# Performance work log

Measured on AMD Instinct MI355X. Metric: run time of the kernel, lower is better.

Reference implementation:

```python
import jax, jax.numpy as jnp
import numpy as np

B, N, D = 2, 1024, 1024
H = 4
KD = 512          # key_dim = d_model * 0.5
VD = 1024         # value_dim = d_model
DK = KD // H      # 128 head_qk_dim
DV = VD // H      # 256 head_v_dim
LR = 16           # gate_low_rank_dim
GLN = 16.0        # gate_logit_normalizer
EPS = 1e-5


def setup_inputs() -> dict:
    key = jax.random.key(0)
    ks = jax.random.split(key, 10)
    s = 0.02
    return {
        "x": jax.random.normal(ks[0], (B, N, D), jnp.float32),
        "Wq": jax.random.normal(ks[1], (D, KD), jnp.float32) * s,
        "Wk": jax.random.normal(ks[2], (D, KD), jnp.float32) * s,
        "Wv": jax.random.normal(ks[3], (D, VD), jnp.float32) * s,
        "Wg": jax.random.normal(ks[4], (D, VD), jnp.float32) * s,
        "Wgk1": jax.random.normal(ks[5], (D, LR), jnp.float32) * s,
        "Wgk2": jax.random.normal(ks[6], (LR, KD), jnp.float32) * s,
        "bgk2": jax.random.normal(ks[7], (KD,), jnp.float32) * s,
        "Wout": jax.random.normal(ks[8], (VD, D), jnp.float32) * s,
        "rms_w": jnp.ones((DV,), jnp.float32),
    }


def _split_heads(t, h):
    b, n, hd = t.shape
    return t.reshape(b, n, h, hd // h).transpose(0, 2, 1, 3)  # b h n d


def _gla_scan(q, k, v, g):
    # q,k: [b,h,n,dk]; v: [b,h,n,dv]; g: [b,h,n,dk] (log-decay)
    b, h, n, dk = q.shape
    dv = v.shape[-1]
    qT = jnp.moveaxis(q, 2, 0)  # [n,b,h,dk]
    kT = jnp.moveaxis(k, 2, 0)
    vT = jnp.moveaxis(v, 2, 0)
    gT = jnp.moveaxis(g, 2, 0)

    def step(S, inp):
        qt, kt, vt, gt = inp
        # S_t = diag(exp(g_t)) S_{t-1} + k_t v_t^T ; o_t = q_t S_t
        S = S * jnp.exp(gt)[..., None] + kt[..., None] * vt[..., None, :]
        ot = jnp.einsum('bhk,bhkv->bhv', qt, S)
        return S, ot

    S0 = jnp.zeros((b, h, dk, dv), q.dtype)
    _, o = jax.lax.scan(step, S0, (qT, kT, vT, gT))
    return jnp.moveaxis(o, 0, 2)  # [b,h,n,dv]


def reference(x, Wq, Wk, Wv, Wg, Wgk1, Wgk2, bgk2, Wout, rms_w):
    q = _split_heads(x @ Wq, H)
    k = _split_heads(x @ Wk, H)
    v = _split_heads(x @ Wv, H)
    g = jax.nn.log_sigmoid((x @ Wgk1) @ Wgk2 + bgk2) / GLN
    g = jnp.maximum(g, -3.0)  # chunk mode clamp
    g = _split_heads(g, H)
    o = _gla_scan(q, k, v, g)               # [b,h,n,dv]
    o = o.transpose(0, 2, 1, 3)             # [b,n,h,dv]
    # RMSNorm over head_v_dim
    o = o * jax.lax.rsqrt(jnp.mean(o * o, axis=-1, keepdims=True) + EPS) * rms_w
    o = o.reshape(o.shape[0], o.shape[1], VD)
    o = o * jax.nn.silu(x @ Wg)
    return o @ Wout
```

## Files before the change

### kernel.cpp

```cpp
#include <hip/hip_runtime.h>
#include <math.h>


typedef __attribute__((ext_vector_type(4))) float vf4;
typedef __attribute__((ext_vector_type(4))) unsigned int vu4;
typedef __attribute__((ext_vector_type(8))) short short8;

#define DEVI static __device__ __forceinline__
DEVI vf4 vzero() { vf4 x = {0.f, 0.f, 0.f, 0.f}; return x; }

DEVI float bf2f(unsigned int u) {
  union { unsigned int i; float f; } c; c.i = u << 16; return c.f;
}
DEVI unsigned short f2bf(float f) {
  union { float f; unsigned int i; } c; c.f = f;
  unsigned int i = c.i;
  return (unsigned short)((i + 0x7fffu + ((i >> 16) & 1u)) >> 16);
}
DEVI void unpack8(vu4 r, float* f) {
  f[0] = bf2f(r.x & 0xffffu); f[1] = bf2f(r.x >> 16);
  f[2] = bf2f(r.y & 0xffffu); f[3] = bf2f(r.y >> 16);
  f[4] = bf2f(r.z & 0xffffu); f[5] = bf2f(r.z >> 16);
  f[6] = bf2f(r.w & 0xffffu); f[7] = bf2f(r.w >> 16);
}
DEVI vu4 pack8(const float* f) {
  vu4 o;
  o.x = (unsigned int)f2bf(f[0]) | ((unsigned int)f2bf(f[1]) << 16);
  o.y = (unsigned int)f2bf(f[2]) | ((unsigned int)f2bf(f[3]) << 16);
  o.z = (unsigned int)f2bf(f[4]) | ((unsigned int)f2bf(f[5]) << 16);
  o.w = (unsigned int)f2bf(f[6]) | ((unsigned int)f2bf(f[7]) << 16);
  return o;
}

__global__ __launch_bounds__(256)
void prep_k(const float* __restrict__ Wq, const float* __restrict__ Wk,
            const float* __restrict__ Wv, const float* __restrict__ Wg,
            const float* __restrict__ Wo, const float* __restrict__ X,
            unsigned short* __restrict__ wqT, unsigned short* __restrict__ wkT,
            unsigned short* __restrict__ wvT, unsigned short* __restrict__ wgT,
            unsigned short* __restrict__ woT, unsigned short* __restrict__ xb) {
  __shared__ float T[64][65];
  const int ct = blockIdx.x, kt = blockIdx.y;
  const int t = threadIdx.x;
  const int r = t >> 2, s = t & 3;
  if (ct >= 64) {
    const int rt = ct - 64;
    const size_t base = (size_t)(rt * 64 + r) * 1024 + kt * 64 + s * 16;
    float f[16];
    *(vf4*)&f[0]  = *(const vf4*)(X + base);
    *(vf4*)&f[4]  = *(const vf4*)(X + base + 4);
    *(vf4*)&f[8]  = *(const vf4*)(X + base + 8);
    *(vf4*)&f[12] = *(const vf4*)(X + base + 12);
    *(vu4*)(xb + base) = pack8(f);
    *(vu4*)(xb + base + 8) = pack8(f + 8);
    return;
  }
  const float* W; unsigned short* O; int N; int cb;
  if (ct < 8)       { W = Wq; O = wqT; N = 512;  cb = ct; }
  else if (ct < 16) { W = Wk; O = wkT; N = 512;  cb = ct - 8; }
  else if (ct < 32) { W = Wv; O = wvT; N = 1024; cb = ct - 16; }
  else if (ct < 48) { W = Wg; O = wgT; N = 1024; cb = ct - 32; }
  else              { W = Wo; O = woT; N = 1024; cb = ct - 48; }
  const float* src = W + (size_t)(kt * 64 + r) * N + cb * 64 + s * 16;
#pragma unroll
  for (int u = 0; u < 4; ++u) {
    vf4 v4 = *(const vf4*)(src + u * 4);
    T[r][s * 16 + u * 4 + 0] = v4.x;
    T[r][s * 16 + u * 4 + 1] = v4.y;
    T[r][s * 16 + u * 4 + 2] = v4.z;
    T[r][s * 16 + u * 4 + 3] = v4.w;
  }
  __syncthreads();
  unsigned int pk[8];
#pragma unroll
  for (int u = 0; u < 8; ++u) {
    unsigned int lo = f2bf(T[s * 16 + 2 * u][r]);
    unsigned int hi = f2bf(T[s * 16 + 2 * u + 1][r]);
    pk[u] = lo | (hi << 16);
  }
  unsigned short* dst = O + (size_t)(cb * 64 + r) * 1024 + kt * 64 + s * 16;
  *(vu4*)dst = *(vu4*)&pk[0];
  *(vu4*)(dst + 8) = *(vu4*)&pk[4];
}

__global__ __launch_bounds__(256)
void proj_mfma_k(const unsigned short* __restrict__ xb,
                 const unsigned short* __restrict__ wqT, const unsigned short* __restrict__ wkT,
                 const unsigned short* __restrict__ wvT, const unsigned short* __restrict__ wgT,
                 unsigned short* __restrict__ qb, unsigned short* __restrict__ kb,
                 unsigned short* __restrict__ vb, unsigned short* __restrict__ sgb) {
  __shared__ __align__(16) unsigned short As[64 * 72];
  __shared__ __align__(16) unsigned short Bs[128 * 72];
  const int t = threadIdx.x;
  const int m0 = blockIdx.y << 6;
  const int nt = blockIdx.x;
  const unsigned short* WT; int n0; int kind;
  if (nt < 4)       { WT = wqT; n0 = nt * 128;        kind = 0; }
  else if (nt < 8)  { WT = wkT; n0 = (nt - 4) * 128;  kind = 1; }
  else if (nt < 16) { WT = wvT; n0 = (nt - 8) * 128;  kind = 2; }
  else              { WT = wgT; n0 = (nt - 16) * 128; kind = 3; }

  const int w = t >> 6, lane = t & 63;
  const int wm = (w >> 1) * 32, wn = (w & 1) * 64;
  const int qd = lane >> 4, m = lane & 15;

  vf4 acc[2][4];
#pragma unroll
  for (int i = 0; i < 2; ++i)
#pragma unroll
    for (int j = 0; j < 4; ++j) acc[i][j] = vzero();

  for (int k0 = 0; k0 < 1024; k0 += 64) {
    __syncthreads();
#pragma unroll
    for (int u2 = 0; u2 < 2; ++u2) {
      const int id = t + (u2 << 8);
      const int row = id >> 3, kg = id & 7;
      vu4 ra = *(const vu4*)(xb + (size_t)(m0 + row) * 1024 + k0 + kg * 8);
      *(vu4*)&As[row * 72 + kg * 8] = ra;
    }
#pragma unroll
    for (int u2 = 0; u2 < 4; ++u2) {
      const int id = t + (u2 << 8);
      const int row = id >> 3, kg = id & 7;
      vu4 rb = *(const vu4*)(WT + (size_t)(n0 + row) * 1024 + k0 + kg * 8);
      *(vu4*)&Bs[row * 72 + kg * 8] = rb;
    }
    __syncthreads();
#pragma unroll
    for (int ks = 0; ks < 2; ++ks) {
      short8 af[2], bf[4];
#pragma unroll
      for (int i = 0; i < 2; ++i)
        af[i] = *(const short8*)&As[(wm + i * 16 + m) * 72 + ks * 32 + qd * 8];
#pragma unroll
      for (int j = 0; j < 4; ++j)
        bf[j] = *(const short8*)&Bs[(wn + j * 16 + m) * 72 + ks * 32 + qd * 8];
#pragma unroll
      for (int i = 0; i < 2; ++i)
#pragma unroll
        for (int j = 0; j < 4; ++j)
          acc[i][j] = __builtin_amdgcn_mfma_f32_16x16x32_bf16(af[i], bf[j], acc[i][j], 0, 0, 0);
    }
  }
#pragma unroll
  for (int i = 0; i < 2; ++i) {
#pragma unroll
    for (int j = 0; j < 4; ++j) {
#pragma unroll
      for (int r = 0; r < 4; ++r) {
        const int grow = m0 + wm + i * 16 + qd * 4 + r;
        const int gcol = n0 + wn + j * 16 + m;
        float val = acc[i][j][r];
        if (kind == 0)      qb[(size_t)grow * 512 + gcol] = f2bf(val);
        else if (kind == 1) kb[(size_t)grow * 512 + gcol] = f2bf(val);
        else if (kind == 2) vb[(size_t)grow * 1024 + gcol] = f2bf(val);
        else {
          val = val / (1.f + expf(-val));
          sgb[(size_t)grow * 1024 + gcol] = f2bf(val);
        }
      }
    }
  }
}

__global__ __launch_bounds__(256)
void out_mfma_k(const unsigned short* __restrict__ Ab,
                const unsigned short* __restrict__ woT, float* __restrict__ Y) {
  __shared__ __align__(16) unsigned short As[64 * 72];
  __shared__ __align__(16) unsigned short Bs[128 * 72];
  const int t = threadIdx.x;
  const int m0 = blockIdx.y << 6;
  const int n0 = blockIdx.x << 7;
  const int w = t >> 6, lane = t & 63;
  const int wm = (w >> 1) * 32, wn = (w & 1) * 64;
  const int qd = lane >> 4, m = lane & 15;

  vf4 acc[2][4];
#pragma unroll
  for (int i = 0; i < 2; ++i)
#pragma unroll
    for (int j = 0; j < 4; ++j) acc[i][j] = vzero();

  for (int k0 = 0; k0 < 1024; k0 += 64) {
    __syncthreads();
#pragma unroll
    for (int u2 = 0; u2 < 2; ++u2) {
      const int id = t + (u2 << 8);
      const int row = id >> 3, kg = id & 7;
      vu4 ra = *(const vu4*)(Ab + (size_t)(m0 + row) * 1024 + k0 + kg * 8);
      *(vu4*)&As[row * 72 + kg * 8] = ra;
    }
#pragma unroll
    for (int u2 = 0; u2 < 4; ++u2) {
      const int id = t + (u2 << 8);
      const int row = id >> 3, kg = id & 7;
      vu4 rb = *(const vu4*)(woT + (size_t)(n0 + row) * 1024 + k0 + kg * 8);
      *(vu4*)&Bs[row * 72 + kg * 8] = rb;
    }
    __syncthreads();
#pragma unroll
    for (int ks = 0; ks < 2; ++ks) {
      short8 af[2], bf[4];
#pragma unroll
      for (int i = 0; i < 2; ++i)
        af[i] = *(const short8*)&As[(wm + i * 16 + m) * 72 + ks * 32 + qd * 8];
#pragma unroll
      for (int j = 0; j < 4; ++j)
        bf[j] = *(const short8*)&Bs[(wn + j * 16 + m) * 72 + ks * 32 + qd * 8];
#pragma unroll
      for (int i = 0; i < 2; ++i)
#pragma unroll
        for (int j = 0; j < 4; ++j)
          acc[i][j] = __builtin_amdgcn_mfma_f32_16x16x32_bf16(af[i], bf[j], acc[i][j], 0, 0, 0);
    }
  }
#pragma unroll
  for (int i = 0; i < 2; ++i)
#pragma unroll
    for (int j = 0; j < 4; ++j)
#pragma unroll
      for (int r = 0; r < 4; ++r) {
        const int grow = m0 + wm + i * 16 + qd * 4 + r;
        const int gcol = n0 + wn + j * 16 + m;
        Y[(size_t)grow * 1024 + gcol] = acc[i][j][r];
      }
}

__global__ __launch_bounds__(64)
void lowrank_k(const float* __restrict__ X, const float* __restrict__ W1,
               float* __restrict__ xl) {
  const int row = blockIdx.x;
  const int t = threadIdx.x;
  float acc[16];
#pragma unroll
  for (int c2 = 0; c2 < 16; ++c2) acc[c2] = 0.f;
  const float* xp = X + (size_t)row * 1024 + t * 16;
  float xv[16];
#pragma unroll
  for (int u = 0; u < 4; ++u)
    *(vf4*)&xv[u * 4] = *(const vf4*)(xp + u * 4);
#pragma unroll
  for (int j = 0; j < 16; ++j) {
    const float* wp = W1 + (size_t)(t * 16 + j) * 16;
    float wv[16];
#pragma unroll
    for (int u = 0; u < 4; ++u)
      *(vf4*)&wv[u * 4] = *(const vf4*)(wp + u * 4);
#pragma unroll
    for (int c2 = 0; c2 < 16; ++c2) acc[c2] = fmaf(xv[j], wv[c2], acc[c2]);
  }
#pragma unroll
  for (int mm = 1; mm < 64; mm <<= 1) {
#pragma unroll
    for (int c2 = 0; c2 < 16; ++c2) acc[c2] += __shfl_xor(acc[c2], mm, 64);
  }
  if (t == 0) {
#pragma unroll
    for (int c2 = 0; c2 < 16; ++c2) xl[(size_t)row * 16 + c2] = acc[c2];
  }
}

__global__ __launch_bounds__(256)
void gate_scan_k(const float* __restrict__ xl, const float* __restrict__ W2,
                 const float* __restrict__ bias,
                 unsigned short* __restrict__ q, unsigned short* __restrict__ k,
                 float* __restrict__ ebtot) {
  const int t = threadIdx.x;
  const int w = t >> 6, lane = t & 63;
  const int wid = blockIdx.x * 4 + w;
  const int kt = wid & 31;
  const int c = (wid >> 5) & 15;
  const int b = wid >> 9;
  const int kbase = kt * 16;
  const size_t rowbase = (size_t)b * 1024 + c * 64;

  const float* xp = xl + (rowbase + lane) * 16;
  float xv[16];
#pragma unroll
  for (int u = 0; u < 4; ++u)
    *(vf4*)&xv[u * 4] = *(const vf4*)(xp + u * 4);

  const size_t a = (rowbase + lane) * 512 + kbase;
  vu4 qr0 = *(const vu4*)(q + a), qr1 = *(const vu4*)(q + a + 8);
  vu4 kr0 = *(const vu4*)(k + a), kr1 = *(const vu4*)(k + a + 8);
  float qf[16], kf[16];
  unpack8(qr0, qf); unpack8(qr1, qf + 8);
  unpack8(kr0, kf); unpack8(kr1, kf + 8);

  float gf[16];
#pragma unroll
  for (int cc = 0; cc < 16; ++cc) {
    const int col = kbase + cc;
    float z = bias[col];
#pragma unroll
    for (int j = 0; j < 16; ++j) z = fmaf(xv[j], W2[j * 512 + col], z);
    float ls = fminf(z, 0.f) - log1pf(expf(-fabsf(z)));
    float g = fmaxf(ls * (1.f / 16.f), -3.f);
#pragma unroll
    for (int d = 1; d < 64; d <<= 1) {
      float up = __shfl_up(g, d, 64);
      if (lane >= d) g += up;
    }
    qf[cc] *= expf(g);
    kf[cc] *= expf(fminf(-g, 80.f));
    gf[cc] = g;
  }
  *(vu4*)(q + a) = pack8(qf);
  *(vu4*)(q + a + 8) = pack8(qf + 8);
  *(vu4*)(k + a) = pack8(kf);
  *(vu4*)(k + a + 8) = pack8(kf + 8);
  if (lane == 63) {
    float* ep = ebtot + ((size_t)b * 16 + c) * 512 + kbase;
#pragma unroll
    for (int cc = 0; cc < 16; ++cc) ep[cc] = expf(gf[cc]);
  }
}

__global__ __launch_bounds__(256)
void intra_kv_k(const unsigned short* __restrict__ q16, const unsigned short* __restrict__ k16,
                const unsigned short* __restrict__ v, float* __restrict__ o,
                unsigned short* __restrict__ ST) {
  __shared__ __align__(16) unsigned short Qs[64 * 136];
  __shared__ __align__(16) unsigned short Ks[64 * 136];
  __shared__ __align__(16) unsigned short Kt[128 * 68];
  __shared__ __align__(16) unsigned short Vt[128 * 68];
  __shared__ __align__(16) unsigned short Asb[64 * 68];
  const int t = threadIdx.x;
  const int vh = blockIdx.x, c = blockIdx.y, bh = blockIdx.z;
  const int b = bh >> 2, h = bh & 3;
  const size_t rowbase = (size_t)b * 1024 + c * 64;

#pragma unroll
  for (int u2 = 0; u2 < 4; ++u2) {
    const int id = t + (u2 << 8);
    const int row = id >> 4, kg = id & 15;
    vu4 rq = *(const vu4*)(q16 + (rowbase + row) * 512 + h * 128 + kg * 8);
    *(vu4*)&Qs[row * 136 + kg * 8] = rq;
    vu4 rk = *(const vu4*)(k16 + (rowbase + row) * 512 + h * 128 + kg * 8);
    *(vu4*)&Ks[row * 136 + kg * 8] = rk;
    const unsigned short* kp = (const unsigned short*)&rk;
#pragma unroll
    for (int u = 0; u < 8; ++u)
      Kt[(kg * 8 + u) * 68 + row] = kp[u];
    vu4 rv = *(const vu4*)(v + (rowbase + row) * 1024 + h * 256 + vh * 128 + kg * 8);
    const unsigned short* vp = (const unsigned short*)&rv;
#pragma unroll
    for (int u = 0; u < 8; ++u)
      Vt[(kg * 8 + u) * 68 + row] = vp[u];
  }
  __syncthreads();

  const int w = t >> 6, lane = t & 63;
  const int qd = lane >> 4, m = lane & 15;

  {
    short8 af[4];
#pragma unroll
    for (int kf = 0; kf < 4; ++kf)
      af[kf] = *(const short8*)&Qs[(w * 16 + m) * 136 + kf * 32 + qd * 8];
    vf4 acc[4];
#pragma unroll
    for (int jt = 0; jt < 4; ++jt) acc[jt] = vzero();
#pragma unroll
    for (int jt = 0; jt < 4; ++jt)
#pragma unroll
      for (int kf = 0; kf < 4; ++kf) {
        short8 bfr = *(const short8*)&Ks[(jt * 16 + m) * 136 + kf * 32 + qd * 8];
        acc[jt] = __builtin_amdgcn_mfma_f32_16x16x32_bf16(af[kf], bfr, acc[jt], 0, 0, 0);
      }
#pragma unroll
    for (int jt = 0; jt < 4; ++jt)
#pragma unroll
      for (int r = 0; r < 4; ++r) {
        const int i = w * 16 + qd * 4 + r;
        const int j = jt * 16 + m;
        Asb[i * 68 + j] = f2bf((j <= i) ? acc[jt][r] : 0.f);
      }
  }
  __syncthreads();

  {
    vf4 acc2[4][2];
#pragma unroll
    for (int mt = 0; mt < 4; ++mt) { acc2[mt][0] = vzero(); acc2[mt][1] = vzero(); }
#pragma unroll
    for (int kf = 0; kf < 2; ++kf) {
      short8 bf0 = *(const short8*)&Vt[(w * 32 + m) * 68 + kf * 32 + qd * 8];
      short8 bf1 = *(const short8*)&Vt[(w * 32 + 16 + m) * 68 + kf * 32 + qd * 8];
#pragma unroll
      for (int mt = 0; mt < 4; ++mt) {
        short8 af = *(const short8*)&Asb[(mt * 16 + m) * 68 + kf * 32 + qd * 8];
        acc2[mt][0] = __builtin_amdgcn_mfma_f32_16x16x32_bf16(af, bf0, acc2[mt][0], 0, 0, 0);
        acc2[mt][1] = __builtin_amdgcn_mfma_f32_16x16x32_bf16(af, bf1, acc2[mt][1], 0, 0, 0);
      }
    }
#pragma unroll
    for (int mt = 0; mt < 4; ++mt)
#pragma unroll
      for (int nt = 0; nt < 2; ++nt)
#pragma unroll
        for (int r = 0; r < 4; ++r) {
          const int i = mt * 16 + qd * 4 + r;
          const int vc = h * 256 + vh * 128 + w * 32 + nt * 16 + m;
          o[(rowbase + i) * 1024 + vc] = acc2[mt][nt][r];
        }
  }

  {
    short8 af3[2][2];
#pragma unroll
    for (int mt = 0; mt < 2; ++mt)
#pragma unroll
      for (int kf = 0; kf < 2; ++kf)
        af3[mt][kf] = *(const short8*)&Vt[(w * 32 + mt * 16 + m) * 68 + kf * 32 + qd * 8];
#pragma unroll
    for (int nt = 0; nt < 8; ++nt) {
      vf4 a0 = vzero(), a1 = vzero();
#pragma unroll
      for (int kf = 0; kf < 2; ++kf) {
        short8 bfr = *(const short8*)&Kt[(nt * 16 + m) * 68 + kf * 32 + qd * 8];
        a0 = __builtin_amdgcn_mfma_f32_16x16x32_bf16(af3[0][kf], bfr, a0, 0, 0, 0);
        a1 = __builtin_amdgcn_mfma_f32_16x16x32_bf16(af3[1][kf], bfr, a1, 0, 0, 0);
      }
      const size_t sbase = (size_t)(bh * 16 + c) * 256 + vh * 128 + w * 32;
#pragma unroll
      for (int r = 0; r < 4; ++r) {
        ST[(sbase + qd * 4 + r) * 128 + nt * 16 + m] = f2bf(a0[r]);
        ST[(sbase + 16 + qd * 4 + r) * 128 + nt * 16 + m] = f2bf(a1[r]);
      }
    }
  }
}

__global__ __launch_bounds__(256)
void state_scan_k(unsigned short* __restrict__ ST, const float* __restrict__ ebtot) {
  const int idx = blockIdx.x * 256 + threadIdx.x;
  const int kg = idx & 15;
  const int vv = (idx >> 4) & 255;
  const int bh = idx >> 12;
  const int b = bh >> 2, h = bh & 3;
  float s[8];
#pragma unroll
  for (int u = 0; u < 8; ++u) s[u] = 0.f;
  for (int c = 0; c < 16; ++c) {
    unsigned short* p = ST + ((size_t)(bh * 16 + c) * 256 + vv) * 128 + kg * 8;
    const float* ep = ebtot + ((size_t)b * 16 + c) * 512 + h * 128 + kg * 8;
    float e[8];
    *(vf4*)&e[0] = *(const vf4*)ep;
    *(vf4*)&e[4] = *(const vf4*)(ep + 4);
    float kv[8];
    unpack8(*(const vu4*)p, kv);
    *(vu4*)p = pack8(s);
#pragma unroll
    for (int u = 0; u < 8; ++u) s[u] = (s[u] + kv[u]) * e[u];
  }
}

__global__ __launch_bounds__(256)
void o_inter_k(const unsigned short* __restrict__ q16, const unsigned short* __restrict__ ST,
               float* __restrict__ o) {
  __shared__ __align__(16) unsigned short Qs[64 * 136];
  __shared__ __align__(16) unsigned short Ss[128 * 136];
  const int t = threadIdx.x;
  const int vt = blockIdx.x, c = blockIdx.y, bh = blockIdx.z;
  const int b = bh >> 2, h = bh & 3;
  const size_t rowbase = (size_t)b * 1024 + c * 64;

#pragma unroll
  for (int u2 = 0; u2 < 4; ++u2) {
    const int id = t + (u2 << 8);
    const int row = id >> 4, kg = id & 15;
    *(vu4*)&Qs[row * 136 + kg * 8] =
        *(const vu4*)(q16 + (rowbase + row) * 512 + h * 128 + kg * 8);
  }
#pragma unroll
  for (int u2 = 0; u2 < 8; ++u2) {
    const int id = t + (u2 << 8);
    const int vrow = id >> 4, kg = id & 15;
    *(vu4*)&Ss[vrow * 136 + kg * 8] =
        *(const vu4*)(ST + ((size_t)(bh * 16 + c) * 256 + vt * 128 + vrow) * 128 + kg * 8);
  }
  __syncthreads();

  const int w = t >> 6, lane = t & 63;
  const int qd = lane >> 4, m = lane & 15;
  short8 af[4];
#pragma unroll
  for (int kf = 0; kf < 4; ++kf)
    af[kf] = *(const short8*)&Qs[(w * 16 + m) * 136 + kf * 32 + qd * 8];
#pragma unroll
  for (int nt = 0; nt < 8; ++nt) {
    vf4 acc = vzero();
#pragma unroll
    for (int kf = 0; kf < 4; ++kf) {
      short8 bfr = *(const short8*)&Ss[(nt * 16 + m) * 136 + kf * 32 + qd * 8];
      acc = __builtin_amdgcn_mfma_f32_16x16x32_bf16(af[kf], bfr, acc, 0, 0, 0);
    }
    float* base = o + (rowbase + w * 16 + qd * 4) * 1024 + h * 256 + vt * 128 + nt * 16 + m;
#pragma unroll
    for (int r = 0; r < 4; ++r)
      base[(size_t)r * 1024] += acc[r];
  }
}

__global__ __launch_bounds__(256)
void norm_gate_k(const float* __restrict__ o, const float* __restrict__ rmsw,
                 const unsigned short* __restrict__ sg,
                 unsigned short* __restrict__ ob) {
  __shared__ float red[4];
  const int grp = blockIdx.x;
  const int row = grp >> 2, h = grp & 3;
  const int t = threadIdx.x;
  const size_t idx = (size_t)row * 1024 + h * 256 + t;
  const float val = o[idx];
  float ss = val * val;
#pragma unroll
  for (int mm = 1; mm < 64; mm <<= 1) ss += __shfl_xor(ss, mm, 64);
  if ((t & 63) == 0) red[t >> 6] = ss;
  __syncthreads();
  const float tot = red[0] + red[1] + red[2] + red[3];
  const float scale = rsqrtf(tot * (1.f / 256.f) + 1e-5f);
  ob[idx] = f2bf(val * scale * rmsw[t] * bf2f((unsigned int)sg[idx]));
}

extern "C" void kernel_launch(void* const* d_in, const int* in_sizes, int n_in,
                              void* d_out, int out_size, void* d_ws, size_t ws_size,
                              hipStream_t stream) {
  const float* x    = (const float*)d_in[0];
  const float* Wq   = (const float*)d_in[1];
  const float* Wk   = (const float*)d_in[2];
  const float* Wv   = (const float*)d_in[3];
  const float* Wg   = (const float*)d_in[4];
  const float* Wgk1 = (const float*)d_in[5];
  const float* Wgk2 = (const float*)d_in[6];
  const float* bgk2 = (const float*)d_in[7];
  const float* Wout = (const float*)d_in[8];
  const float* rmsw = (const float*)d_in[9];

  const size_t MB = 1u << 20;
  char* w = (char*)d_ws;
  unsigned short* qb16   = (unsigned short*)(w);
  unsigned short* kb16   = (unsigned short*)(w + 2 * MB);
  unsigned short* vbuf   = (unsigned short*)(w + 4 * MB);
  unsigned short* sgbuf  = (unsigned short*)(w + 8 * MB);
  float*          obuf   = (float*)(w + 12 * MB);
  char*           sreg   = w + 20 * MB;
  unsigned short* xb     = (unsigned short*)sreg;
  unsigned short* STbuf  = (unsigned short*)sreg;
  unsigned short* obuf_b = (unsigned short*)sreg;
  float*          xlbuf  = (float*)(w + 28 * MB);
  float*          ebbuf  = (float*)(w + 28 * MB + 131072);
  unsigned short* wqT    = (unsigned short*)(w + 29 * MB);
  unsigned short* wkT    = (unsigned short*)(w + 30 * MB);
  unsigned short* wvT    = (unsigned short*)(w + 31 * MB);
  unsigned short* wgT    = (unsigned short*)(w + 33 * MB);
  unsigned short* woT    = (unsigned short*)(w + 35 * MB);

  prep_k<<<dim3(96, 16), 256, 0, stream>>>(Wq, Wk, Wv, Wg, Wout, x,
                                           wqT, wkT, wvT, wgT, woT, xb);
  lowrank_k<<<2048, 64, 0, stream>>>(x, Wgk1, xlbuf);
  proj_mfma_k<<<dim3(24, 32), 256, 0, stream>>>(xb, wqT, wkT, wvT, wgT, qb16, kb16, vbuf, sgbuf);
  gate_scan_k<<<256, 256, 0, stream>>>(xlbuf, Wgk2, bgk2, qb16, kb16, ebbuf);
  intra_kv_k<<<dim3(2, 16, 8), 256, 0, stream>>>(qb16, kb16, vbuf, obuf, STbuf);
  state_scan_k<<<128, 256, 0, stream>>>(STbuf, ebbuf);
  o_inter_k<<<dim3(2, 16, 8), 256, 0, stream>>>(qb16, STbuf, obuf);
  norm_gate_k<<<8192, 256, 0, stream>>>(obuf, rmsw, sgbuf, obuf_b);
  out_mfma_k<<<dim3(8, 32), 256, 0, stream>>>(obuf_b, woT, (float*)d_out);
}
```

Baseline: 192.3 us.

## Use direct global-to-LDS loads with XOR swizzle and larger projection GEMM tile

Both the projection and output GEMMs now stage tiles with global_load_lds 16-byte direct-to-LDS loads instead of going through VGPRs. The padded LDS layout is replaced by an XOR-swizzled 64-wide layout to avoid bank conflicts. The projection GEMM tile grows from 64x128 to 128x128 with a 4x4 accumulator array per wave, halving the grid. This aims to cut register traffic and raise data reuse, at the cost of more registers per wave and fewer blocks for the projection kernel.

New measurement: 194.2 us. Within noise of the previous version (+1.0%).

```diff
diff --git a/kernel.cpp b/kernel.cpp
--- a/kernel.cpp
+++ b/kernel.cpp
@@ -30,6 +30,13 @@
   o.z = (unsigned int)f2bf(f[4]) | ((unsigned int)f2bf(f[5]) << 16);
   o.w = (unsigned int)f2bf(f[6]) | ((unsigned int)f2bf(f[7]) << 16);
   return o;
+}
+
+DEVI void gld16(const unsigned short* g, unsigned short* l) {
+  __builtin_amdgcn_global_load_lds(
+      (const __attribute__((address_space(1))) unsigned int*)g,
+      (__attribute__((address_space(3))) unsigned int*)l,
+      16, 0, 0);
 }
 
 __global__ __launch_bounds__(256)
@@ -89,62 +96,58 @@
                  const unsigned short* __restrict__ wvT, const unsigned short* __restrict__ wgT,
                  unsigned short* __restrict__ qb, unsigned short* __restrict__ kb,
                  unsigned short* __restrict__ vb, unsigned short* __restrict__ sgb) {
-  __shared__ __align__(16) unsigned short As[64 * 72];
-  __shared__ __align__(16) unsigned short Bs[128 * 72];
-  const int t = threadIdx.x;
-  const int m0 = blockIdx.y << 6;
+  __shared__ __align__(16) unsigned short As[128 * 64];
+  __shared__ __align__(16) unsigned short Bs[128 * 64];
+  const int t = threadIdx.x;
+  const int m0 = blockIdx.y << 7;
   const int nt = blockIdx.x;
   const unsigned short* WT; int n0; int kind;
-  if (nt < 4)       { WT = wqT; n0 = nt * 128;        kind = 0; }
-  else if (nt < 8)  { WT = wkT; n0 = (nt - 4) * 128;  kind = 1; }
-  else if (nt < 16) { WT = wvT; n0 = (nt - 8) * 128;  kind = 2; }
-  else              { WT = wgT; n0 = (nt - 16) * 128; kind = 3; }
+  if (nt < 4)       { WT = wqT; n0 = nt << 7;        kind = 0; }
+  else if (nt < 8)  { WT = wkT; n0 = (nt - 4) << 7;  kind = 1; }
+  else if (nt < 16) { WT = wvT; n0 = (nt - 8) << 7;  kind = 2; }
+  else              { WT = wgT; n0 = (nt - 16) << 7; kind = 3; }
 
   const int w = t >> 6, lane = t & 63;
-  const int wm = (w >> 1) * 32, wn = (w & 1) * 64;
+  const int wm = (w >> 1) << 6, wn = (w & 1) << 6;
   const int qd = lane >> 4, m = lane & 15;
-
-  vf4 acc[2][4];
-#pragma unroll
-  for (int i = 0; i < 2; ++i)
+  const int srow = lane >> 3;
+  const int scol = ((lane & 7) ^ srow) << 3;
+
+  vf4 acc[4][4];
+#pragma unroll
+  for (int i = 0; i < 4; ++i)
 #pragma unroll
     for (int j = 0; j < 4; ++j) acc[i][j] = vzero();
 
   for (int k0 = 0; k0 < 1024; k0 += 64) {
     __syncthreads();
 #pragma unroll
-    for (int u2 = 0; u2 < 2; ++u2) {
-      const int id = t + (u2 << 8);
-      const int row = id >> 3, kg = id & 7;
-      vu4 ra = *(const vu4*)(xb + (size_t)(m0 + row) * 1024 + k0 + kg * 8);
-      *(vu4*)&As[row * 72 + kg * 8] = ra;
-    }
-#pragma unroll
-    for (int u2 = 0; u2 < 4; ++u2) {
-      const int id = t + (u2 << 8);
-      const int row = id >> 3, kg = id & 7;
-      vu4 rb = *(const vu4*)(WT + (size_t)(n0 + row) * 1024 + k0 + kg * 8);
-      *(vu4*)&Bs[row * 72 + kg * 8] = rb;
+    for (int cc = 0; cc < 4; ++cc) {
+      const int c = (w << 2) + cc;
+      const int row = (c << 3) + srow;
+      gld16(xb + (size_t)(m0 + row) * 1024 + k0 + scol, (unsigned short*)As + (c << 9));
+      gld16(WT + (size_t)(n0 + row) * 1024 + k0 + scol, (unsigned short*)Bs + (c << 9));
     }
     __syncthreads();
 #pragma unroll
     for (int ks = 0; ks < 2; ++ks) {
-      short8 af[2], bf[4];
-#pragma unroll
-      for (int i = 0; i < 2; ++i)
-        af[i] = *(const short8*)&As[(wm + i * 16 + m) * 72 + ks * 32 + qd * 8];
+      const int sw = (((ks << 2) + qd) ^ (m & 7)) << 3;
+      short8 af[4], bf[4];
+#pragma unroll
+      for (int i = 0; i < 4; ++i)
+        af[i] = *(const short8*)&As[(wm + i * 16 + m) * 64 + sw];
 #pragma unroll
       for (int j = 0; j < 4; ++j)
-        bf[j] = *(const short8*)&Bs[(wn + j * 16 + m) * 72 + ks * 32 + qd * 8];
-#pragma unroll
-      for (int i = 0; i < 2; ++i)
+        bf[j] = *(const short8*)&Bs[(wn + j * 16 + m) * 64 + sw];
+#pragma unroll
+      for (int i = 0; i < 4; ++i)
 #pragma unroll
         for (int j = 0; j < 4; ++j)
           acc[i][j] = __builtin_amdgcn_mfma_f32_16x16x32_bf16(af[i], bf[j], acc[i][j], 0, 0, 0);
     }
   }
 #pragma unroll
-  for (int i = 0; i < 2; ++i) {
+  for (int i = 0; i < 4; ++i) {
 #pragma unroll
     for (int j = 0; j < 4; ++j) {
 #pragma unroll
@@ -167,14 +170,16 @@
 __global__ __launch_bounds__(256)
 void out_mfma_k(const unsigned short* __restrict__ Ab,
                 const unsigned short* __restrict__ woT, float* __restrict__ Y) {
-  __shared__ __align__(16) unsigned short As[64 * 72];
-  __shared__ __align__(16) unsigned short Bs[128 * 72];
+  __shared__ __align__(16) unsigned short As[64 * 64];
+  __shared__ __align__(16) unsigned short Bs[128 * 64];
   const int t = threadIdx.x;
   const int m0 = blockIdx.y << 6;
   const int n0 = blockIdx.x << 7;
   const int w = t >> 6, lane = t & 63;
   const int wm = (w >> 1) * 32, wn = (w & 1) * 64;
   const int qd = lane >> 4, m = lane & 15;
+  const int srow = lane >> 3;
+  const int scol = ((lane & 7) ^ srow) << 3;
 
   vf4 acc[2][4];
 #pragma unroll
@@ -185,29 +190,28 @@
   for (int k0 = 0; k0 < 1024; k0 += 64) {
     __syncthreads();
 #pragma unroll
-    for (int u2 = 0; u2 < 2; ++u2) {
-      const int id = t + (u2 << 8);
-      const int row = id >> 3, kg = id & 7;
-      vu4 ra = *(const vu4*)(Ab + (size_t)(m0 + row) * 1024 + k0 + kg * 8);
-      *(vu4*)&As[row * 72 + kg * 8] = ra;
-    }
-#pragma unroll
-    for (int u2 = 0; u2 < 4; ++u2) {
-      const int id = t + (u2 << 8);
-      const int row = id >> 3, kg = id & 7;
-      vu4 rb = *(const vu4*)(woT + (size_t)(n0 + row) * 1024 + k0 + kg * 8);
-      *(vu4*)&Bs[row * 72 + kg * 8] = rb;
+    for (int cc = 0; cc < 2; ++cc) {
+      const int c = (w << 1) + cc;
+      const int row = (c << 3) + srow;
+      gld16(Ab + (size_t)(m0 + row) * 1024 + k0 + scol, (unsigned short*)As + (c << 9));
+    }
+#pragma unroll
+    for (int cc = 0; cc < 4; ++cc) {
+      const int c = (w << 2) + cc;
+      const int row = (c << 3) + srow;
+      gld16(woT + (size_t)(n0 + row) * 1024 + k0 + scol, (unsigned short*)Bs + (c << 9));
     }
     __syncthreads();
 #pragma unroll
     for (int ks = 0; ks < 2; ++ks) {
+      const int sw = (((ks << 2) + qd) ^ (m & 7)) << 3;
       short8 af[2], bf[4];
 #pragma unroll
       for (int i = 0; i < 2; ++i)
-        af[i] = *(const short8*)&As[(wm + i * 16 + m) * 72 + ks * 32 + qd * 8];
+        af[i] = *(const short8*)&As[(wm + i * 16 + m) * 64 + sw];
 #pragma unroll
       for (int j = 0; j < 4; ++j)
-        bf[j] = *(const short8*)&Bs[(wn + j * 16 + m) * 72 + ks * 32 + qd * 8];
+        bf[j] = *(const short8*)&Bs[(wn + j * 16 + m) * 64 + sw];
 #pragma unroll
       for (int i = 0; i < 2; ++i)
 #pragma unroll
@@ -560,7 +564,7 @@
   prep_k<<<dim3(96, 16), 256, 0, stream>>>(Wq, Wk, Wv, Wg, Wout, x,
                                            wqT, wkT, wvT, wgT, woT, xb);
   lowrank_k<<<2048, 64, 0, stream>>>(x, Wgk1, xlbuf);
-  proj_mfma_k<<<dim3(24, 32), 256, 0, stream>>>(xb, wqT, wkT, wvT, wgT, qb16, kb16, vbuf, sgbuf);
+  proj_mfma_k<<<dim3(24, 16), 256, 0, stream>>>(xb, wqT, wkT, wvT, wgT, qb16, kb16, vbuf, sgbuf);
   gate_scan_k<<<256, 256, 0, stream>>>(xlbuf, Wgk2, bgk2, qb16, kb16, ebbuf);
   intra_kv_k<<<dim3(2, 16, 8), 256, 0, stream>>>(qb16, kb16, vbuf, obuf, STbuf);
   state_scan_k<<<128, 256, 0, stream>>>(STbuf, ebbuf);
```
